# Kernel optimization log

Hardware: AMD Instinct MI355X
Metric: run time of the kernel (lower is better)

## Reference

```python
import math
import jax, jax.numpy as jnp
import numpy as np

D_MODEL = 1024
N_HEADS = 16
D_FF = 4096
B = 4
T = 1024  # tgt len
S = 1024  # src len
EPS = 1e-6


def _linear_params(key, d_in, d_out):
    kw, kb = jax.random.split(key)
    w = jax.random.normal(kw, (d_out, d_in), dtype=jnp.float32) * 0.02
    b = jax.random.normal(kb, (d_out,), dtype=jnp.float32) * 0.02
    return w, b


def setup_inputs() -> dict:
    key = jax.random.key(0)
    ks = jax.random.split(key, 16)
    x = jax.random.normal(ks[0], (B, T, D_MODEL), dtype=jnp.float32)
    memory = jax.random.normal(ks[1], (B, S, D_MODEL), dtype=jnp.float32)
    # causal [B, T, T] mask (dim==3 branch) and padding [B, S] mask (dim==2 branch)
    tgt_mask = jnp.broadcast_to(jnp.tril(jnp.ones((T, T), dtype=jnp.int32)), (B, T, T))
    src_mask = jnp.ones((B, S), dtype=jnp.int32)
    inp = {"x": x, "memory": memory, "tgt_mask": tgt_mask, "src_mask": src_mask}
    names = ["sa_wq", "sa_wk", "sa_wv", "sa_wo", "ca_wq", "ca_wk", "ca_wv", "ca_wo"]
    for i, n in enumerate(names):
        w, b = _linear_params(ks[2 + i], D_MODEL, D_MODEL)
        inp[n] = w
        inp[n.replace("w", "b")] = b
    inp["ff_w1"], inp["ff_b1"] = _linear_params(ks[10], D_MODEL, D_FF)
    inp["ff_w2"], inp["ff_b2"] = _linear_params(ks[11], D_FF, D_MODEL)
    for i, n in enumerate(["ln1", "ln2", "ln3"]):
        inp[n + "_w"] = jnp.ones((D_MODEL,), dtype=jnp.float32)
        inp[n + "_b"] = jnp.zeros((D_MODEL,), dtype=jnp.float32)
    return inp


def layernorm(x, w, b):
    # torch-faithful: unbiased std (N-1), eps added to std (not variance)
    mean = jnp.mean(x, axis=-1, keepdims=True)
    d = x - mean
    std = jnp.sqrt(jnp.sum(d * d, axis=-1, keepdims=True) / (x.shape[-1] - 1))
    return w * d / (std + EPS) + b


def mha(q_in, kv_in, mask, wq, bq, wk, bk, wv, bv, wo, bo):
    Bb, Tq, D = q_in.shape
    Tk = kv_in.shape[1]
    dk = D // N_HEADS
    if mask.ndim == 2:
        mask4 = mask[:, None, None, :]
    else:
        mask4 = mask[:, None, :, :]
    q = (q_in @ wq.T + bq).reshape(Bb, Tq, N_HEADS, dk).transpose(0, 2, 1, 3)
    k = (kv_in @ wk.T + bk).reshape(Bb, Tk, N_HEADS, dk).transpose(0, 2, 1, 3)
    v = (kv_in @ wv.T + bv).reshape(Bb, Tk, N_HEADS, dk).transpose(0, 2, 1, 3)
    scores = jnp.einsum("bhqd,bhkd->bhqk", q, k) / math.sqrt(dk)
    scores = jnp.where(mask4 == 0, jnp.float32(-1e9), scores)
    attn = jax.nn.softmax(scores, axis=-1)
    out = jnp.einsum("bhqk,bhkd->bhqd", attn, v)
    out = out.transpose(0, 2, 1, 3).reshape(Bb, Tq, D)
    return out @ wo.T + bo


def reference(x, memory, tgt_mask, src_mask,
              sa_wq, sa_bq, sa_wk, sa_bk, sa_wv, sa_bv, sa_wo, sa_bo,
              ca_wq, ca_bq, ca_wk, ca_bk, ca_wv, ca_bv, ca_wo, ca_bo,
              ff_w1, ff_b1, ff_w2, ff_b2,
              ln1_w, ln1_b, ln2_w, ln2_b, ln3_w, ln3_b):
    # pre-norm decoder block (norm_first=True), dropout=0 (eval)
    h = layernorm(x, ln1_w, ln1_b)
    x = x + mha(h, h, tgt_mask, sa_wq, sa_bq, sa_wk, sa_bk, sa_wv, sa_bv, sa_wo, sa_bo)
    h = layernorm(x, ln2_w, ln2_b)
    x = x + mha(h, memory, src_mask, ca_wq, ca_bq, ca_wk, ca_bk, ca_wv, ca_bv, ca_wo, ca_bo)
    h = layernorm(x, ln3_w, ln3_b)
    x = x + (jax.nn.relu(h @ ff_w1.T + ff_b1) @ ff_w2.T + ff_b2)
    return x
```

## Files before the change

### kernel.cpp

```cpp
#include <hip/hip_runtime.h>
#include <hip/hip_bf16.h>

typedef unsigned short u16;
typedef __attribute__((ext_vector_type(4))) float f32x4;
typedef __attribute__((ext_vector_type(8))) short s16x8;
typedef __attribute__((ext_vector_type(4))) short s16x4;
typedef __attribute__((ext_vector_type(8))) __bf16 bf16x8;

#define NTOK 4096
#define DMODEL 1024
#define DFF 4096
#define NH 16
#define TSEQ 1024


__device__ __forceinline__ u16 f2bu(float f) {
  unsigned int u = __float_as_uint(f);
  unsigned int r = (u + 0x7FFFu + ((u >> 16) & 1u)) >> 16;
  return (u16)r;
}

__device__ __forceinline__ f32x4 mfma16(s16x8 a, s16x8 b, f32x4 c) {
  return __builtin_amdgcn_mfma_f32_16x16x32_bf16((bf16x8)a, (bf16x8)b, c, 0, 0, 0);
}

__device__ __forceinline__ void gload16(const u16* g, u16* l) {
  __builtin_amdgcn_global_load_lds(
      (const __attribute__((address_space(1))) unsigned int*)g,
      (__attribute__((address_space(3))) unsigned int*)l, 16, 0, 0);
}

__device__ __forceinline__ s16x8 ldfrag(const u16* p) {
  s16x4 lo = *(const s16x4*)p;
  s16x4 hi = *(const s16x4*)(p + 16);
  s16x8 r;
  r[0] = lo[0]; r[1] = lo[1]; r[2] = lo[2]; r[3] = lo[3];
  r[4] = hi[0]; r[5] = hi[1]; r[6] = hi[2]; r[7] = hi[3];
  return r;
}

__device__ __forceinline__ s16x8 ld8s(const u16* t, int row, int eoff) {
  int rx = row & 7;
  const u16* p1 = t + row * 64 + ((((eoff >> 3) ^ rx) << 3) | (eoff & 7));
  const u16* p2 = t + row * 64 + (((((eoff + 16) >> 3) ^ rx) << 3) | (eoff & 7));
  s16x4 lo = *(const s16x4*)p1;
  s16x4 hi = *(const s16x4*)p2;
  s16x8 r;
  r[0] = lo[0]; r[1] = lo[1]; r[2] = lo[2]; r[3] = lo[3];
  r[4] = hi[0]; r[5] = hi[1]; r[6] = hi[2]; r[7] = hi[3];
  return r;
}

__device__ __forceinline__ s16x8 ld16s(const u16* t, int row, int ch) {
  return *(const s16x8*)(t + row * 64 + ((ch ^ (row & 7)) << 3));
}


struct F2B {
  const float* s[11];
  u16* d[11];
};

__global__ __launch_bounds__(256) void f2b_all(F2B a) {
  int bid = blockIdx.x;
  int seg, boff;
  if (bid < 8192) { seg = bid >> 10; boff = bid & 1023; }
  else { int j = bid - 8192; seg = 8 + (j >> 12); boff = j & 4095; }
  size_t i = ((size_t)boff * 256 + threadIdx.x) * 4;
  float4 v = *(const float4*)(a.s[seg] + i);
  ushort4 o = make_ushort4(f2bu(v.x), f2bu(v.y), f2bu(v.z), f2bu(v.w));
  *(ushort4*)(a.d[seg] + i) = o;
}


__global__ __launch_bounds__(256) void ln_kernel(const float* __restrict__ x,
                                                 const float* __restrict__ w,
                                                 const float* __restrict__ b,
                                                 u16* __restrict__ out) {
  int row = blockIdx.x;
  int t = threadIdx.x;
  const float* xr = x + (size_t)row * DMODEL;
  float4 v = *(const float4*)(xr + t * 4);
  float s = v.x + v.y + v.z + v.w;
#pragma unroll
  for (int off = 1; off < 64; off <<= 1) s += __shfl_xor(s, off);
  __shared__ float red[8];
  int wid = t >> 6, lane = t & 63;
  if (lane == 0) red[wid] = s;
  __syncthreads();
  float mean = (red[0] + red[1] + red[2] + red[3]) * (1.0f / 1024.0f);
  float dx = v.x - mean, dy = v.y - mean, dz = v.z - mean, dw = v.w - mean;
  float ss = dx * dx + dy * dy + dz * dz + dw * dw;
#pragma unroll
  for (int off = 1; off < 64; off <<= 1) ss += __shfl_xor(ss, off);
  if (lane == 0) red[4 + wid] = ss;
  __syncthreads();
  float sst = red[4] + red[5] + red[6] + red[7];
  float inv = 1.0f / (sqrtf(sst / 1023.0f) + 1e-6f);
  float4 wv = *(const float4*)(w + t * 4);
  float4 bv = *(const float4*)(b + t * 4);
  ushort4 o = make_ushort4(f2bu(wv.x * dx * inv + bv.x), f2bu(wv.y * dy * inv + bv.y),
                           f2bu(wv.z * dz * inv + bv.z), f2bu(wv.w * dw * inv + bv.w));
  *(ushort4*)(out + (size_t)row * DMODEL + t * 4) = o;
}


template <int MODE, bool RELU, bool SPLITK = false>
__global__ __launch_bounds__(512) void gemm_bt(const u16* __restrict__ A,
                                               const u16* __restrict__ W,
                                               const float* __restrict__ b0,
                                               const float* __restrict__ b1,
                                               const float* __restrict__ b2,
                                               const float* resid, void* outp,
                                               int M, int N, int K, int ld,
                                               int gx) {
  __shared__ u16 As[2][128 * 64];
  __shared__ u16 Bs[2][128 * 64];
  const int nwg = gridDim.x;
  const int qch = nwg >> 3;
  const int bid = blockIdx.x;
  int wg = (bid & 7) * qch + (bid >> 3);
  int half = 0;
  if (SPLITK) { half = wg & 1; wg >>= 1; }
  const int bx = wg % gx, by = wg / gx;
  const int m0 = by * 128, n0 = bx * 128;
  if (SPLITK) { A += (size_t)half * K; W += (size_t)half * K; }
  const int tid = threadIdx.x;
  const int wid = tid >> 6, lane = tid & 63;
  const int wr = wid >> 2, wc = wid & 3;
  const int lhi = lane >> 4, llo = lane & 15;
  f32x4 acc[4][2] = {};
  const int sr = tid >> 3, sc = tid & 7;
  const int srcoff = (sc ^ (sr & 7)) << 3;

  auto stage = [&](int kk, int buf) {
    const u16* Ap = A + (size_t)(m0 + sr) * ld + kk + srcoff;
    gload16(Ap, &As[buf][tid * 8]);
    gload16(Ap + (size_t)64 * ld, &As[buf][4096 + tid * 8]);
    const u16* Wp = W + (size_t)(n0 + sr) * ld + kk + srcoff;
    gload16(Wp, &Bs[buf][tid * 8]);
    gload16(Wp + (size_t)64 * ld, &Bs[buf][4096 + tid * 8]);
  };

  stage(0, 0);
  __syncthreads();

  for (int k0 = 0; k0 < K; k0 += 64) {
    int cur = (k0 >> 6) & 1;
    if (k0 + 64 < K) stage(k0 + 64, cur ^ 1);
#pragma unroll
    for (int ks8 = 0; ks8 < 8; ks8 += 4) {
      s16x8 af[4], bfr[2];
#pragma unroll
      for (int f = 0; f < 4; f++) af[f] = ld16s(&As[cur][0], wr * 64 + f * 16 + llo, ks8 + lhi);
#pragma unroll
      for (int g = 0; g < 2; g++) bfr[g] = ld16s(&Bs[cur][0], wc * 32 + g * 16 + llo, ks8 + lhi);
#pragma unroll
      for (int f = 0; f < 4; f++)
#pragma unroll
        for (int g = 0; g < 2; g++) acc[f][g] = mfma16(af[f], bfr[g], acc[f][g]);
    }
    __syncthreads();
  }

  const float* bias;
  if (MODE == 2) {
    int bs = n0 >> 10;
    bias = (bs == 0) ? b0 : ((bs == 1) ? b1 : b2);
  } else {
    bias = b0;
  }

#pragma unroll
  for (int fm = 0; fm < 4; fm++) {
#pragma unroll
    for (int fn = 0; fn < 2; fn++) {
      int c = n0 + wc * 32 + fn * 16 + llo;
      float bv = bias ? (MODE == 2 ? bias[c & 1023] : bias[c]) : 0.0f;
#pragma unroll
      for (int i = 0; i < 4; i++) {
        int r = m0 + wr * 64 + fm * 16 + lhi * 4 + i;
        float v = acc[fm][fn][i] + bv;
        if (resid) v += resid[(size_t)r * N + c];
        if (RELU) v = fmaxf(v, 0.0f);
        if (MODE == 0) {
          ((float*)outp)[(size_t)half * M * N + (size_t)r * N + c] = v;
        } else if (MODE == 1) {
          ((u16*)outp)[(size_t)r * N + c] = f2bu(v);
        } else {
          int buf = c >> 10, cc = c & 1023;
          int bb = r >> 10, t = r & 1023, hh = cc >> 6, d = cc & 63;
          ((u16*)outp)[(size_t)buf * 4194304 +
                       (((size_t)(bb * NH + hh)) * TSEQ + t) * 64 + d] = f2bu(v);
        }
      }
    }
  }
}


__global__ __launch_bounds__(256) void ff2_reduce(const float* __restrict__ p,
                                                  const float* __restrict__ bias,
                                                  float* __restrict__ out) {
  int row = blockIdx.x, t = threadIdx.x;
  size_t i = (size_t)row * 1024 + t * 4;
  const float* p1 = p + (size_t)4194304;
  float4 a = *(const float4*)(p + i);
  float4 b = *(const float4*)(p1 + i);
  float4 r = *(const float4*)(out + i);
  float4 bv = *(const float4*)(bias + t * 4);
  float4 o = make_float4(a.x + b.x + r.x + bv.x, a.y + b.y + r.y + bv.y,
                         a.z + b.z + r.z + bv.z, a.w + b.w + r.w + bv.w);
  *(float4*)(out + i) = o;
}


template <bool CAUSAL>
__global__ __launch_bounds__(256) void attn_kernel(const u16* __restrict__ Qg,
                                                   const u16* __restrict__ Kg,
                                                   const u16* __restrict__ Vg,
                                                   u16* __restrict__ Og) {
  int bh = blockIdx.y;
  int b = bh >> 4, h = bh & 15;
  int q0 = blockIdx.x * 128;
  int tid = threadIdx.x, wid = tid >> 6, lane = tid & 63;
  int lhi = lane >> 4, llo = lane & 15;
  __shared__ u16 Ks[2][4096];
  __shared__ u16 Vs[2][4096];

  int qr = q0 + wid * 16 + llo;
  const u16* qp0 = Qg + ((size_t)bh * TSEQ + qr) * 64;
  const u16* qp1 = qp0 + 64 * 64;
  s16x8 qf[2][2];
  qf[0][0] = ldfrag(qp0 + lhi * 4);
  qf[0][1] = ldfrag(qp0 + 32 + lhi * 4);
  qf[1][0] = ldfrag(qp1 + lhi * 4);
  qf[1][1] = ldfrag(qp1 + 32 + lhi * 4);

  f32x4 oacc[2][4] = {};
  float mrun[2] = {-3.0e38f, -3.0e38f}, lrun[2] = {0.0f, 0.0f};
  const size_t kvbase = (size_t)bh * TSEQ * 64;
  const int nt = (CAUSAL ? (q0 + 128) : TSEQ) >> 6;

  const int kr = tid >> 3, kc = tid & 7;
  const int ksrc = (kc ^ (kr & 7)) << 3;
  const int vkv = tid & 63, vd0 = (tid >> 6) * 8;
  s16x8 vr0, vr1;

  auto stageK = [&](int s0, int buf) {
    const u16* kb = Kg + kvbase + (size_t)s0 * 64;
    gload16(kb + (size_t)kr * 64 + ksrc, &Ks[buf][tid * 8]);
    gload16(kb + (size_t)(32 + kr) * 64 + ksrc, &Ks[buf][2048 + tid * 8]);
  };
  auto loadV = [&](int s0) {
    const u16* vb = Vg + kvbase + (size_t)(s0 + vkv) * 64;
    vr0 = *(const s16x8*)(vb + vd0);
    vr1 = *(const s16x8*)(vb + vd0 + 32);
  };
  auto writeV = [&](int buf) {
#pragma unroll
    for (int j = 0; j < 8; j++) {
      int d = vd0 + j;
      Vs[buf][d * 64 + ((((vkv >> 3) ^ (d & 7)) << 3) | (vkv & 7))] = (u16)vr0[j];
      int d2 = d + 32;
      Vs[buf][d2 * 64 + ((((vkv >> 3) ^ (d2 & 7)) << 3) | (vkv & 7))] = (u16)vr1[j];
    }
  };

  stageK(0, 0);
  loadV(0);
  writeV(0);
  __syncthreads();

  for (int t = 0; t < nt; ++t) {
    int cur = t & 1;
    if (t + 1 < nt) {
      stageK((t + 1) * 64, cur ^ 1);
      loadV((t + 1) * 64);
    }
    int s0 = t * 64;
    const bool act0 = !CAUSAL || (s0 < q0 + 64);

    s16x8 kf[4][2];
#pragma unroll
    for (int g = 0; g < 4; g++) {
      int row = g * 16 + llo;
      kf[g][0] = ld8s(&Ks[cur][0], row, lhi * 4);
      kf[g][1] = ld8s(&Ks[cur][0], row, 32 + lhi * 4);
    }

    s16x8 pf[2][2];
#pragma unroll
    for (int s = 0; s < 2; s++) {
      if (s == 0 && !act0) continue;
      f32x4 sacc[4] = {};
#pragma unroll
      for (int g = 0; g < 4; g++) {
        sacc[g] = mfma16(kf[g][0], qf[s][0], sacc[g]);
        sacc[g] = mfma16(kf[g][1], qf[s][1], sacc[g]);
      }
      int qrow = qr + s * 64;
      float sv[16];
      float pmax = -3.0e38f;
#pragma unroll
      for (int g = 0; g < 4; g++)
#pragma unroll
        for (int i = 0; i < 4; i++) {
          float sc = sacc[g][i] * 0.125f;
          if (CAUSAL) {
            int kv = s0 + g * 16 + lhi * 4 + i;
            if (kv > qrow) sc = -1.0e9f;
          }
          sv[g * 4 + i] = sc;
          pmax = fmaxf(pmax, sc);
        }
      pmax = fmaxf(pmax, __shfl_xor(pmax, 16));
      pmax = fmaxf(pmax, __shfl_xor(pmax, 32));
      float mnew = fmaxf(mrun[s], pmax);
      float alpha = __expf(mrun[s] - mnew);
      float ls = 0.0f;
#pragma unroll
      for (int j = 0; j < 16; j++) {
        float p = __expf(sv[j] - mnew);
        sv[j] = p;
        ls += p;
      }
      ls += __shfl_xor(ls, 16);
      ls += __shfl_xor(ls, 32);
      lrun[s] = lrun[s] * alpha + ls;
      mrun[s] = mnew;
#pragma unroll
      for (int g = 0; g < 4; g++) {
        oacc[s][g][0] *= alpha; oacc[s][g][1] *= alpha;
        oacc[s][g][2] *= alpha; oacc[s][g][3] *= alpha;
      }
#pragma unroll
      for (int kk = 0; kk < 2; kk++)
#pragma unroll
        for (int i2 = 0; i2 < 8; i2++)
          pf[s][kk][i2] = (short)f2bu(sv[(kk * 2 + (i2 >> 2)) * 4 + (i2 & 3)]);
    }

#pragma unroll
    for (int dg = 0; dg < 4; dg++) {
      int row = dg * 16 + llo;
      s16x8 vf0 = ld8s(&Vs[cur][0], row, lhi * 4);
      s16x8 vf1 = ld8s(&Vs[cur][0], row, 32 + lhi * 4);
#pragma unroll
      for (int s = 0; s < 2; s++) {
        if (s == 0 && !act0) continue;
        oacc[s][dg] = mfma16(vf0, pf[s][0], oacc[s][dg]);
        oacc[s][dg] = mfma16(vf1, pf[s][1], oacc[s][dg]);
      }
    }

    if (t + 1 < nt) writeV(cur ^ 1);
    __syncthreads();
  }

#pragma unroll
  for (int s = 0; s < 2; s++) {
    float inv = 1.0f / lrun[s];
    u16* orow = Og + (size_t)(b * TSEQ + qr + s * 64) * DMODEL + h * 64;
#pragma unroll
    for (int dg = 0; dg < 4; dg++)
#pragma unroll
      for (int i = 0; i < 4; i++)
        orow[dg * 16 + lhi * 4 + i] = f2bu(oacc[s][dg][i] * inv);
  }
}


extern "C" void kernel_launch(void* const* d_in, const int* in_sizes, int n_in,
                              void* d_out, int out_size, void* d_ws, size_t ws_size,
                              hipStream_t stream) {
  const float* x      = (const float*)d_in[0];
  const float* memory = (const float*)d_in[1];
  const float* sa_wq = (const float*)d_in[4];  const float* sa_bq = (const float*)d_in[5];
  const float* sa_wk = (const float*)d_in[6];  const float* sa_bk = (const float*)d_in[7];
  const float* sa_wv = (const float*)d_in[8];  const float* sa_bv = (const float*)d_in[9];
  const float* sa_wo = (const float*)d_in[10]; const float* sa_bo = (const float*)d_in[11];
  const float* ca_wq = (const float*)d_in[12]; const float* ca_bq = (const float*)d_in[13];
  const float* ca_wk = (const float*)d_in[14]; const float* ca_bk = (const float*)d_in[15];
  const float* ca_wv = (const float*)d_in[16]; const float* ca_bv = (const float*)d_in[17];
  const float* ca_wo = (const float*)d_in[18]; const float* ca_bo = (const float*)d_in[19];
  const float* ff_w1 = (const float*)d_in[20]; const float* ff_b1 = (const float*)d_in[21];
  const float* ff_w2 = (const float*)d_in[22]; const float* ff_b2 = (const float*)d_in[23];
  const float* ln1_w = (const float*)d_in[24]; const float* ln1_b = (const float*)d_in[25];
  const float* ln2_w = (const float*)d_in[26]; const float* ln2_b = (const float*)d_in[27];
  const float* ln3_w = (const float*)d_in[28]; const float* ln3_b = (const float*)d_in[29];
  float* out = (float*)d_out;

  char* ws = (char*)d_ws;
  const size_t MB = 1u << 20;
  u16* h_bf   = (u16*)(ws + 0 * MB);
  u16* mem_bf = (u16*)(ws + 8 * MB);
  u16* qb     = (u16*)(ws + 16 * MB);
  u16* kb     = (u16*)(ws + 24 * MB);
  u16* vb     = (u16*)(ws + 32 * MB);
  u16* attnb  = (u16*)(ws + 40 * MB);
  u16* ffmid  = (u16*)(ws + 48 * MB);
  float* pk   = (float*)(ws + 16 * MB);
  u16* w_sq   = (u16*)(ws + 80 * MB);
  u16* w_sk   = (u16*)(ws + 82 * MB);
  u16* w_sv   = (u16*)(ws + 84 * MB);
  u16* w_so   = (u16*)(ws + 86 * MB);
  u16* w_cq   = (u16*)(ws + 88 * MB);
  u16* w_ck   = (u16*)(ws + 90 * MB);
  u16* w_cv   = (u16*)(ws + 92 * MB);
  u16* w_co   = (u16*)(ws + 94 * MB);
  u16* w_f1   = (u16*)(ws + 96 * MB);
  u16* w_f2   = (u16*)(ws + 104 * MB);

  F2B fa;
  fa.s[0] = sa_wq; fa.d[0] = w_sq;
  fa.s[1] = sa_wk; fa.d[1] = w_sk;
  fa.s[2] = sa_wv; fa.d[2] = w_sv;
  fa.s[3] = sa_wo; fa.d[3] = w_so;
  fa.s[4] = ca_wq; fa.d[4] = w_cq;
  fa.s[5] = ca_wk; fa.d[5] = w_ck;
  fa.s[6] = ca_wv; fa.d[6] = w_cv;
  fa.s[7] = ca_wo; fa.d[7] = w_co;
  fa.s[8] = ff_w1; fa.d[8] = w_f1;
  fa.s[9] = ff_w2; fa.d[9] = w_f2;
  fa.s[10] = memory; fa.d[10] = mem_bf;
  f2b_all<<<20480, 256, 0, stream>>>(fa);

  dim3 gattn(8, 64);

  ln_kernel<<<4096, 256, 0, stream>>>(x, ln1_w, ln1_b, h_bf);
  gemm_bt<2, false><<<768, 512, 0, stream>>>(h_bf, w_sq, sa_bq, sa_bk, sa_bv,
                                             nullptr, qb, NTOK, 3072, DMODEL, DMODEL, 24);
  attn_kernel<true><<<gattn, 256, 0, stream>>>(qb, kb, vb, attnb);
  gemm_bt<0, false><<<256, 512, 0, stream>>>(attnb, w_so, sa_bo, nullptr, nullptr,
                                             x, out, NTOK, DMODEL, DMODEL, DMODEL, 8);

  ln_kernel<<<4096, 256, 0, stream>>>(out, ln2_w, ln2_b, h_bf);
  gemm_bt<2, false><<<256, 512, 0, stream>>>(h_bf, w_cq, ca_bq, nullptr, nullptr,
                                             nullptr, qb, NTOK, DMODEL, DMODEL, DMODEL, 8);
  gemm_bt<2, false><<<512, 512, 0, stream>>>(mem_bf, w_ck, ca_bk, ca_bv, nullptr,
                                             nullptr, kb, NTOK, 2048, DMODEL, DMODEL, 16);
  attn_kernel<false><<<gattn, 256, 0, stream>>>(qb, kb, vb, attnb);
  gemm_bt<0, false><<<256, 512, 0, stream>>>(attnb, w_co, ca_bo, nullptr, nullptr,
                                             out, out, NTOK, DMODEL, DMODEL, DMODEL, 8);

  ln_kernel<<<4096, 256, 0, stream>>>(out, ln3_w, ln3_b, h_bf);
  gemm_bt<1, true><<<1024, 512, 0, stream>>>(h_bf, w_f1, ff_b1, nullptr, nullptr,
                                             nullptr, ffmid, NTOK, DFF, DMODEL, DMODEL, 32);
  gemm_bt<0, false, true><<<512, 512, 0, stream>>>(ffmid, w_f2, nullptr, nullptr, nullptr,
                                                   nullptr, pk, NTOK, DMODEL, 2048, DFF, 8);
  ff2_reduce<<<4096, 256, 0, stream>>>(pk, ff_b2, out);

  (void)in_sizes; (void)n_in; (void)out_size; (void)ws_size;
}
```

Baseline: 353.9 us.

## Restructure attention to 64-query tiles with direct K loads and lazy rescale

The attention kernel now gives each workgroup 64 query rows instead of 128 and launches a 1D grid of 1024 blocks in an XCD-aware order. K fragments are read directly from global memory instead of being staged through LDS. The online softmax skips the rescale of the running max and accumulator unless the max grows by more than a threshold. Float-to-bf16 conversion now uses the hardware cast in every kernel. These changes aim to raise occupancy and cut LDS traffic and exp work, but they give up K reuse across two query sub-tiles and make each workgroup reload K from global or L2.

```diff
diff --git a/kernel.cpp b/kernel.cpp
--- a/kernel.cpp
+++ b/kernel.cpp
@@ -14,10 +14,10 @@
 #define TSEQ 1024
 
 
-__device__ __forceinline__ u16 f2bu(float f) {
-  unsigned int u = __float_as_uint(f);
-  unsigned int r = (u + 0x7FFFu + ((u >> 16) & 1u)) >> 16;
-  return (u16)r;
+__device__ __forceinline__ u16 f2b_hw(float f) {
+  union { __bf16 h; u16 u; } cv;
+  cv.h = (__bf16)f;
+  return cv.u;
 }
 
 __device__ __forceinline__ f32x4 mfma16(s16x8 a, s16x8 b, f32x4 c) {
@@ -28,15 +28,6 @@
   __builtin_amdgcn_global_load_lds(
       (const __attribute__((address_space(1))) unsigned int*)g,
       (__attribute__((address_space(3))) unsigned int*)l, 16, 0, 0);
-}
-
-__device__ __forceinline__ s16x8 ldfrag(const u16* p) {
-  s16x4 lo = *(const s16x4*)p;
-  s16x4 hi = *(const s16x4*)(p + 16);
-  s16x8 r;
-  r[0] = lo[0]; r[1] = lo[1]; r[2] = lo[2]; r[3] = lo[3];
-  r[4] = hi[0]; r[5] = hi[1]; r[6] = hi[2]; r[7] = hi[3];
-  return r;
 }
 
 __device__ __forceinline__ s16x8 ld8s(const u16* t, int row, int eoff) {
@@ -68,7 +59,7 @@
   else { int j = bid - 8192; seg = 8 + (j >> 12); boff = j & 4095; }
   size_t i = ((size_t)boff * 256 + threadIdx.x) * 4;
   float4 v = *(const float4*)(a.s[seg] + i);
-  ushort4 o = make_ushort4(f2bu(v.x), f2bu(v.y), f2bu(v.z), f2bu(v.w));
+  ushort4 o = make_ushort4(f2b_hw(v.x), f2b_hw(v.y), f2b_hw(v.z), f2b_hw(v.w));
   *(ushort4*)(a.d[seg] + i) = o;
 }
 
@@ -99,8 +90,8 @@
   float inv = 1.0f / (sqrtf(sst / 1023.0f) + 1e-6f);
   float4 wv = *(const float4*)(w + t * 4);
   float4 bv = *(const float4*)(b + t * 4);
-  ushort4 o = make_ushort4(f2bu(wv.x * dx * inv + bv.x), f2bu(wv.y * dy * inv + bv.y),
-                           f2bu(wv.z * dz * inv + bv.z), f2bu(wv.w * dw * inv + bv.w));
+  ushort4 o = make_ushort4(f2b_hw(wv.x * dx * inv + bv.x), f2b_hw(wv.y * dy * inv + bv.y),
+                           f2b_hw(wv.z * dz * inv + bv.z), f2b_hw(wv.w * dw * inv + bv.w));
   *(ushort4*)(out + (size_t)row * DMODEL + t * 4) = o;
 }
 
@@ -186,12 +177,12 @@
         if (MODE == 0) {
           ((float*)outp)[(size_t)half * M * N + (size_t)r * N + c] = v;
         } else if (MODE == 1) {
-          ((u16*)outp)[(size_t)r * N + c] = f2bu(v);
+          ((u16*)outp)[(size_t)r * N + c] = f2b_hw(v);
         } else {
           int buf = c >> 10, cc = c & 1023;
           int bb = r >> 10, t = r & 1023, hh = cc >> 6, d = cc & 63;
           ((u16*)outp)[(size_t)buf * 4194304 +
-                       (((size_t)(bb * NH + hh)) * TSEQ + t) * 64 + d] = f2bu(v);
+                       (((size_t)(bb * NH + hh)) * TSEQ + t) * 64 + d] = f2b_hw(v);
         }
       }
     }
@@ -220,38 +211,28 @@
                                                    const u16* __restrict__ Kg,
                                                    const u16* __restrict__ Vg,
                                                    u16* __restrict__ Og) {
-  int bh = blockIdx.y;
-  int b = bh >> 4, h = bh & 15;
-  int q0 = blockIdx.x * 128;
-  int tid = threadIdx.x, wid = tid >> 6, lane = tid & 63;
-  int lhi = lane >> 4, llo = lane & 15;
-  __shared__ u16 Ks[2][4096];
+  const int bid = blockIdx.x;
+  const int wg = (bid & 7) * 128 + (bid >> 3);
+  const int bh = wg >> 4, qblk = wg & 15;
+  const int b = bh >> 4, h = bh & 15;
+  const int q0 = qblk * 64;
+  const int tid = threadIdx.x, wid = tid >> 6, lane = tid & 63;
+  const int lhi = lane >> 4, llo = lane & 15;
   __shared__ u16 Vs[2][4096];
 
-  int qr = q0 + wid * 16 + llo;
-  const u16* qp0 = Qg + ((size_t)bh * TSEQ + qr) * 64;
-  const u16* qp1 = qp0 + 64 * 64;
-  s16x8 qf[2][2];
-  qf[0][0] = ldfrag(qp0 + lhi * 4);
-  qf[0][1] = ldfrag(qp0 + 32 + lhi * 4);
-  qf[1][0] = ldfrag(qp1 + lhi * 4);
-  qf[1][1] = ldfrag(qp1 + 32 + lhi * 4);
-
-  f32x4 oacc[2][4] = {};
-  float mrun[2] = {-3.0e38f, -3.0e38f}, lrun[2] = {0.0f, 0.0f};
+  const int qr = q0 + wid * 16 + llo;
+  const u16* qp = Qg + ((size_t)bh * TSEQ + qr) * 64;
+  s16x8 qf0 = *(const s16x8*)(qp + 8 * lhi);
+  s16x8 qf1 = *(const s16x8*)(qp + 8 * (4 + lhi));
+
+  f32x4 oacc[4] = {};
+  float mrun = -1.0e30f, lrun = 0.0f;
   const size_t kvbase = (size_t)bh * TSEQ * 64;
-  const int nt = (CAUSAL ? (q0 + 128) : TSEQ) >> 6;
-
-  const int kr = tid >> 3, kc = tid & 7;
-  const int ksrc = (kc ^ (kr & 7)) << 3;
+  const int nt = (CAUSAL ? (q0 + 64) : TSEQ) >> 6;
+
   const int vkv = tid & 63, vd0 = (tid >> 6) * 8;
   s16x8 vr0, vr1;
 
-  auto stageK = [&](int s0, int buf) {
-    const u16* kb = Kg + kvbase + (size_t)s0 * 64;
-    gload16(kb + (size_t)kr * 64 + ksrc, &Ks[buf][tid * 8]);
-    gload16(kb + (size_t)(32 + kr) * 64 + ksrc, &Ks[buf][2048 + tid * 8]);
-  };
   auto loadV = [&](int s0) {
     const u16* vb = Vg + kvbase + (size_t)(s0 + vkv) * 64;
     vr0 = *(const s16x8*)(vb + vd0);
@@ -267,107 +248,89 @@
     }
   };
 
-  stageK(0, 0);
   loadV(0);
   writeV(0);
   __syncthreads();
 
   for (int t = 0; t < nt; ++t) {
     int cur = t & 1;
-    if (t + 1 < nt) {
-      stageK((t + 1) * 64, cur ^ 1);
-      loadV((t + 1) * 64);
-    }
+    if (t + 1 < nt) loadV((t + 1) * 64);
     int s0 = t * 64;
-    const bool act0 = !CAUSAL || (s0 < q0 + 64);
-
-    s16x8 kf[4][2];
+
+    const u16* kb = Kg + kvbase + (size_t)s0 * 64;
+    f32x4 sacc[4] = {};
 #pragma unroll
     for (int g = 0; g < 4; g++) {
-      int row = g * 16 + llo;
-      kf[g][0] = ld8s(&Ks[cur][0], row, lhi * 4);
-      kf[g][1] = ld8s(&Ks[cur][0], row, 32 + lhi * 4);
-    }
-
-    s16x8 pf[2][2];
-#pragma unroll
-    for (int s = 0; s < 2; s++) {
-      if (s == 0 && !act0) continue;
-      f32x4 sacc[4] = {};
+      const u16* kp = kb + (size_t)(g * 16 + llo) * 64;
+      s16x8 k0 = *(const s16x8*)(kp + 8 * lhi);
+      s16x8 k1 = *(const s16x8*)(kp + 8 * (4 + lhi));
+      sacc[g] = mfma16(k0, qf0, sacc[g]);
+      sacc[g] = mfma16(k1, qf1, sacc[g]);
+    }
+
+    float sv[16];
+    float pmax = -1.0e30f;
+#pragma unroll
+    for (int g = 0; g < 4; g++)
+#pragma unroll
+      for (int i = 0; i < 4; i++) {
+        float sc = sacc[g][i] * 0.125f;
+        if (CAUSAL) {
+          int kv = s0 + g * 16 + lhi * 4 + i;
+          if (kv > qr) sc = -1.0e9f;
+        }
+        sv[g * 4 + i] = sc;
+        pmax = fmaxf(pmax, sc);
+      }
+    pmax = fmaxf(pmax, __shfl_xor(pmax, 16));
+    pmax = fmaxf(pmax, __shfl_xor(pmax, 32));
+    if (!__all(pmax - mrun <= 8.0f)) {
+      float mnew = fmaxf(mrun, pmax);
+      float alpha = __expf(mrun - mnew);
+      lrun *= alpha;
 #pragma unroll
       for (int g = 0; g < 4; g++) {
-        sacc[g] = mfma16(kf[g][0], qf[s][0], sacc[g]);
-        sacc[g] = mfma16(kf[g][1], qf[s][1], sacc[g]);
+        oacc[g][0] *= alpha; oacc[g][1] *= alpha;
+        oacc[g][2] *= alpha; oacc[g][3] *= alpha;
       }
-      int qrow = qr + s * 64;
-      float sv[16];
-      float pmax = -3.0e38f;
-#pragma unroll
-      for (int g = 0; g < 4; g++)
-#pragma unroll
-        for (int i = 0; i < 4; i++) {
-          float sc = sacc[g][i] * 0.125f;
-          if (CAUSAL) {
-            int kv = s0 + g * 16 + lhi * 4 + i;
-            if (kv > qrow) sc = -1.0e9f;
-          }
-          sv[g * 4 + i] = sc;
-          pmax = fmaxf(pmax, sc);
-        }
-      pmax = fmaxf(pmax, __shfl_xor(pmax, 16));
-      pmax = fmaxf(pmax, __shfl_xor(pmax, 32));
-      float mnew = fmaxf(mrun[s], pmax);
-      float alpha = __expf(mrun[s] - mnew);
-      float ls = 0.0f;
-#pragma unroll
-      for (int j = 0; j < 16; j++) {
-        float p = __expf(sv[j] - mnew);
-        sv[j] = p;
-        ls += p;
-      }
-      ls += __shfl_xor(ls, 16);
-      ls += __shfl_xor(ls, 32);
-      lrun[s] = lrun[s] * alpha + ls;
-      mrun[s] = mnew;
-#pragma unroll
-      for (int g = 0; g < 4; g++) {
-        oacc[s][g][0] *= alpha; oacc[s][g][1] *= alpha;
-        oacc[s][g][2] *= alpha; oacc[s][g][3] *= alpha;
-      }
-#pragma unroll
-      for (int kk = 0; kk < 2; kk++)
-#pragma unroll
-        for (int i2 = 0; i2 < 8; i2++)
-          pf[s][kk][i2] = (short)f2bu(sv[(kk * 2 + (i2 >> 2)) * 4 + (i2 & 3)]);
-    }
+      mrun = mnew;
+    }
+    float ls = 0.0f;
+#pragma unroll
+    for (int j = 0; j < 16; j++) {
+      float p = __expf(sv[j] - mrun);
+      sv[j] = p;
+      ls += p;
+    }
+    ls += __shfl_xor(ls, 16);
+    ls += __shfl_xor(ls, 32);
+    lrun += ls;
+
+    s16x8 pf[2];
+#pragma unroll
+    for (int kk = 0; kk < 2; kk++)
+#pragma unroll
+      for (int i2 = 0; i2 < 8; i2++)
+        pf[kk][i2] = (short)f2b_hw(sv[(kk * 2 + (i2 >> 2)) * 4 + (i2 & 3)]);
 
 #pragma unroll
     for (int dg = 0; dg < 4; dg++) {
       int row = dg * 16 + llo;
-      s16x8 vf0 = ld8s(&Vs[cur][0], row, lhi * 4);
-      s16x8 vf1 = ld8s(&Vs[cur][0], row, 32 + lhi * 4);
-#pragma unroll
-      for (int s = 0; s < 2; s++) {
-        if (s == 0 && !act0) continue;
-        oacc[s][dg] = mfma16(vf0, pf[s][0], oacc[s][dg]);
-        oacc[s][dg] = mfma16(vf1, pf[s][1], oacc[s][dg]);
-      }
+      oacc[dg] = mfma16(ld8s(&Vs[cur][0], row, lhi * 4), pf[0], oacc[dg]);
+      oacc[dg] = mfma16(ld8s(&Vs[cur][0], row, 32 + lhi * 4), pf[1], oacc[dg]);
     }
 
     if (t + 1 < nt) writeV(cur ^ 1);
     __syncthreads();
   }
 
-#pragma unroll
-  for (int s = 0; s < 2; s++) {
-    float inv = 1.0f / lrun[s];
-    u16* orow = Og + (size_t)(b * TSEQ + qr + s * 64) * DMODEL + h * 64;
-#pragma unroll
-    for (int dg = 0; dg < 4; dg++)
-#pragma unroll
-      for (int i = 0; i < 4; i++)
-        orow[dg * 16 + lhi * 4 + i] = f2bu(oacc[s][dg][i] * inv);
-  }
+  float inv = 1.0f / lrun;
+  u16* orow = Og + (size_t)(b * TSEQ + qr) * DMODEL + h * 64;
+#pragma unroll
+  for (int dg = 0; dg < 4; dg++)
+#pragma unroll
+    for (int i = 0; i < 4; i++)
+      orow[dg * 16 + lhi * 4 + i] = f2b_hw(oacc[dg][i] * inv);
 }
 
 
@@ -426,12 +389,10 @@
   fa.s[10] = memory; fa.d[10] = mem_bf;
   f2b_all<<<20480, 256, 0, stream>>>(fa);
 
-  dim3 gattn(8, 64);
-
   ln_kernel<<<4096, 256, 0, stream>>>(x, ln1_w, ln1_b, h_bf);
   gemm_bt<2, false><<<768, 512, 0, stream>>>(h_bf, w_sq, sa_bq, sa_bk, sa_bv,
                                              nullptr, qb, NTOK, 3072, DMODEL, DMODEL, 24);
-  attn_kernel<true><<<gattn, 256, 0, stream>>>(qb, kb, vb, attnb);
+  attn_kernel<true><<<1024, 256, 0, stream>>>(qb, kb, vb, attnb);
   gemm_bt<0, false><<<256, 512, 0, stream>>>(attnb, w_so, sa_bo, nullptr, nullptr,
                                              x, out, NTOK, DMODEL, DMODEL, DMODEL, 8);
 
@@ -440,7 +401,7 @@
                                              nullptr, qb, NTOK, DMODEL, DMODEL, DMODEL, 8);
   gemm_bt<2, false><<<512, 512, 0, stream>>>(mem_bf, w_ck, ca_bk, ca_bv, nullptr,
                                              nullptr, kb, NTOK, 2048, DMODEL, DMODEL, 16);
-  attn_kernel<false><<<gattn, 256, 0, stream>>>(qb, kb, vb, attnb);
+  attn_kernel<false><<<1024, 256, 0, stream>>>(qb, kb, vb, attnb);
   gemm_bt<0, false><<<256, 512, 0, stream>>>(attnb, w_co, ca_bo, nullptr, nullptr,
                                              out, out, NTOK, DMODEL, DMODEL, DMODEL, 8);
 
```

New measurement: 422.1 us. +19.3%, slower.
